# Kernel tuning notes

Measured on AMD Instinct MI355X. Metric: run time of the kernel, lower is better.

The kernel has to match this reference:

```python
import jax, jax.numpy as jnp
import numpy as np

N_NODES = 100000
N_EDGES = 1600000
DIM = 64          # num_features == hidden_dim
N_LAYERS = 5
N_GRAPHS = 1024
EMB = DIM * N_LAYERS  # 320
BN_EPS = 1e-5


def setup_inputs() -> dict:
    key = jax.random.key(0)
    ks = jax.random.split(key, 16)
    s = 0.05
    return {
        "x": jax.random.normal(ks[0], (N_NODES, DIM), dtype=jnp.float32),
        "edge_index": jax.random.randint(ks[1], (2, N_EDGES), 0, N_NODES, dtype=jnp.int32),
        "edge_weight": jax.random.uniform(ks[2], (N_EDGES,), dtype=jnp.float32),
        "batch": jnp.sort(jax.random.randint(ks[3], (N_NODES,), 0, N_GRAPHS, dtype=jnp.int32)),
        # stacked per-layer GIN MLP params: nn = Linear(d,d) -> ReLU -> Linear(d,d)
        "W1s": jax.random.normal(ks[4], (N_LAYERS, DIM, DIM), dtype=jnp.float32) * s,
        "b1s": jnp.zeros((N_LAYERS, DIM), dtype=jnp.float32),
        "W2s": jax.random.normal(ks[5], (N_LAYERS, DIM, DIM), dtype=jnp.float32) * s,
        "b2s": jnp.zeros((N_LAYERS, DIM), dtype=jnp.float32),
        # BatchNorm1d affine params (init: weight=1, bias=0)
        "gammas": jnp.ones((N_LAYERS, DIM), dtype=jnp.float32),
        "betas": jnp.zeros((N_LAYERS, DIM), dtype=jnp.float32),
        # projection head: Linear(EMB,EMB) -> ReLU -> Linear(EMB,EMB)
        "pW1": jax.random.normal(ks[6], (EMB, EMB), dtype=jnp.float32) * s,
        "pb1": jnp.zeros((EMB,), dtype=jnp.float32),
        "pW2": jax.random.normal(ks[7], (EMB, EMB), dtype=jnp.float32) * s,
        "pb2": jnp.zeros((EMB,), dtype=jnp.float32),
    }


def _encoder(x, src, dst, edge_weight, batch,
             W1s, b1s, W2s, b2s, gammas, betas):
    h = x
    pooled = []
    for i in range(N_LAYERS):
        # WGINConv (eps=0): h_out = nn(h + sum_{j->i} w_ij * h_j)
        msg = jax.ops.segment_sum(h[src] * edge_weight[:, None], dst,
                                  num_segments=N_NODES)  # [N, D]
        z = h + msg
        z = jnp.maximum(z @ W1s[i] + b1s[i], 0.0) @ W2s[i] + b2s[i]
        h = jnp.maximum(z, 0.0)  # F.relu after conv
        # BatchNorm1d (training mode: batch stats over nodes, biased var)
        mean = jnp.mean(h, axis=0)
        var = jnp.var(h, axis=0)
        h = (h - mean) * jax.lax.rsqrt(var + BN_EPS) * gammas[i] + betas[i]
        pooled.append(h)
    # global_mean_pool per layer, then concat along feature dim
    counts = jax.ops.segment_sum(jnp.ones((N_NODES,), h.dtype), batch,
                                 num_segments=N_GRAPHS)
    counts = jnp.maximum(counts, 1.0)[:, None]
    xpool = [jax.ops.segment_sum(h, batch, num_segments=N_GRAPHS) / counts
             for h in pooled]
    return jnp.concatenate(xpool, axis=1)  # [G, L*D]


def reference(x, edge_index, edge_weight, batch,
              W1s, b1s, W2s, b2s, gammas, betas,
              pW1, pb1, pW2, pb2):
    src, dst = edge_index[0], edge_index[1]
    y = _encoder(x, src, dst, edge_weight, batch,
                 W1s, b1s, W2s, b2s, gammas, betas)
    # proj_head: Linear -> ReLU -> Linear
    y = jnp.maximum(y @ pW1 + pb1, 0.0) @ pW2 + pb2
    return y
```

## Files before the change

### kernel.cpp

```cpp
#include <hip/hip_runtime.h>

#define NN 100000
#define NE 1600000
#define D 64
#define NL 5
#define NG 1024
#define EMBD 320
#define BN_EPS 1e-5f
#define SCAN_NB ((NN + 255) / 256)
#define GIN_NB ((NN + 63) / 64)

__global__ __launch_bounds__(256) void k_gbound(const int* __restrict__ batch,
                                                int* __restrict__ gstart) {
  int i = blockIdx.x * 256 + threadIdx.x;
  if (i >= NN) return;
  int b = batch[i];
  int bp = (i == 0) ? -1 : batch[i - 1];
  for (int g = bp + 1; g <= b; ++g) gstart[g] = i;
  if (i == NN - 1) {
    for (int g = b + 1; g <= NG; ++g) gstart[g] = NN;
  }
}

__global__ __launch_bounds__(256) void k_hist(const int* __restrict__ dst,
                                              int* __restrict__ deg) {
  int e = blockIdx.x * 256 + threadIdx.x;
  if (e < NE) atomicAdd(&deg[dst[e]], 1);
}

__global__ __launch_bounds__(256) void k_scan1(const int* __restrict__ deg,
                                               int* __restrict__ bsums) {
  __shared__ int sh[256];
  int i = blockIdx.x * 256 + threadIdx.x;
  sh[threadIdx.x] = (i < NN) ? deg[i] : 0;
  __syncthreads();
  for (int off = 128; off > 0; off >>= 1) {
    if (threadIdx.x < off) sh[threadIdx.x] += sh[threadIdx.x + off];
    __syncthreads();
  }
  if (threadIdx.x == 0) bsums[blockIdx.x] = sh[0];
}

__global__ __launch_bounds__(512) void k_scan2(int* __restrict__ bsums) {
  __shared__ int sh[512];
  int t = threadIdx.x;
  int v = (t < SCAN_NB) ? bsums[t] : 0;
  sh[t] = v;
  __syncthreads();
  for (int off = 1; off < 512; off <<= 1) {
    int u = (t >= off) ? sh[t - off] : 0;
    __syncthreads();
    sh[t] += u;
    __syncthreads();
  }
  if (t < SCAN_NB) bsums[t] = sh[t] - v;
}

__global__ __launch_bounds__(256) void k_scan3(int* __restrict__ row_ptr,
                                               int* __restrict__ cursor,
                                               const int* __restrict__ bsums) {
  __shared__ int sh[256];
  int t = threadIdx.x;
  int i = blockIdx.x * 256 + t;
  int v = (i < NN) ? row_ptr[i] : 0;
  sh[t] = v;
  __syncthreads();
  for (int off = 1; off < 256; off <<= 1) {
    int u = (t >= off) ? sh[t - off] : 0;
    __syncthreads();
    sh[t] += u;
    __syncthreads();
  }
  int excl = sh[t] - v + bsums[blockIdx.x];
  if (i < NN) {
    row_ptr[i] = excl;
    cursor[i] = excl;
    if (i == NN - 1) row_ptr[NN] = excl + v;
  }
}

__global__ __launch_bounds__(256) void k_fill(const int* __restrict__ src,
                                              const int* __restrict__ dst,
                                              const float* __restrict__ w,
                                              int* __restrict__ cursor,
                                              int2* __restrict__ epair) {
  int e = blockIdx.x * 256 + threadIdx.x;
  if (e >= NE) return;
  int slot = atomicAdd(&cursor[dst[e]], 1);
  int2 p;
  p.x = src[e];
  p.y = __float_as_int(w[e]);
  epair[slot] = p;
}

#define FMA4(A, V) \
  A.x = fmaf(V.x, we, A.x); A.y = fmaf(V.y, we, A.y); \
  A.z = fmaf(V.z, we, A.z); A.w = fmaf(V.w, we, A.w);

__global__ __launch_bounds__(256, 4) void k_gin(const float* __restrict__ h,
                                                float* __restrict__ gout,
                                                const int* __restrict__ row_ptr,
                                                const int2* __restrict__ epair,
                                                const float* __restrict__ W1,
                                                const float* __restrict__ b1,
                                                const float* __restrict__ W2,
                                                const float* __restrict__ b2,
                                                const float* __restrict__ statsP,
                                                const float* __restrict__ gammaP,
                                                const float* __restrict__ betaP,
                                                int useaff,
                                                float* __restrict__ statsL) {
  __shared__ float zin[64 * 65];
  __shared__ float sW[64 * 64];
  __shared__ float sb[64];
  __shared__ float wsumS[64];
  __shared__ float scA[64], sbA[64];
  __shared__ float sSf[256], sQf[256];
  const int t = threadIdx.x;
  const int nb = blockIdx.x * 64;
  const int nr = t >> 4, fc = t & 15;

  for (int i = t; i < 4096; i += 256) sW[i] = W1[i];
  if (t < 64) {
    sb[t] = b1[t];
    if (useaff) {
      float m = statsP[t] * (1.f / NN);
      float v = fmaxf(statsP[64 + t] * (1.f / NN) - m * m, 0.f);
      float sc = gammaP[t] * rsqrtf(v + BN_EPS);
      scA[t] = sc;
      sbA[t] = betaP[t] - m * sc;
    }
  }

  {
    const int nl = t >> 2;
    const int q = t & 3;
    const int n = nb + nl;
    float4 a0 = {0.f, 0.f, 0.f, 0.f}, a1 = a0, a2 = a0, a3 = a0;
    float wsum = 0.f;
    if (n < NN) {
      const int beg = row_ptr[n], end = row_ptr[n + 1];
      const float4* own = (const float4*)(h + (size_t)n * D) + q * 4;
      for (int i = beg; i < end; ++i) {
        const int2 pr = epair[i];
        const float we = __int_as_float(pr.y);
        const float4* hp = (const float4*)(h + (size_t)pr.x * D) + q * 4;
        float4 v0 = hp[0], v1 = hp[1], v2 = hp[2], v3 = hp[3];
        FMA4(a0, v0) FMA4(a1, v1) FMA4(a2, v2) FMA4(a3, v3)
        wsum += we;
      }
      float4 o0 = own[0], o1 = own[1], o2 = own[2], o3 = own[3];
      a0.x += o0.x; a0.y += o0.y; a0.z += o0.z; a0.w += o0.w;
      a1.x += o1.x; a1.y += o1.y; a1.z += o1.z; a1.w += o1.w;
      a2.x += o2.x; a2.y += o2.y; a2.z += o2.z; a2.w += o2.w;
      a3.x += o3.x; a3.y += o3.y; a3.z += o3.z; a3.w += o3.w;
    }
    float* zr = &zin[nl * 65 + q * 16];
    *(float4*)(zr + 0) = a0;
    *(float4*)(zr + 4) = a1;
    *(float4*)(zr + 8) = a2;
    *(float4*)(zr + 12) = a3;
    if (q == 0) wsumS[nl] = wsum;
  }
  __syncthreads();

  if (useaff) {
#pragma unroll
    for (int pass = 0; pass < 4; ++pass) {
      int idx = pass * 1024 + t * 4;
      int r = idx >> 6, c = idx & 63;
      float wp1 = 1.f + wsumS[r];
      float4 z = *(float4*)&zin[r * 65 + c];
      z.x = fmaf(z.x, scA[c + 0], sbA[c + 0] * wp1);
      z.y = fmaf(z.y, scA[c + 1], sbA[c + 1] * wp1);
      z.z = fmaf(z.z, scA[c + 2], sbA[c + 2] * wp1);
      z.w = fmaf(z.w, scA[c + 3], sbA[c + 3] * wp1);
      *(float4*)&zin[r * 65 + c] = z;
    }
    __syncthreads();
  }

#define GEMM_TILE(ACC)                                                        \
  {                                                                           \
    float4 bias = *(float4*)&sb[fc * 4];                                      \
    _Pragma("unroll") for (int i = 0; i < 4; ++i) ACC[i] = bias;              \
    _Pragma("unroll 4") for (int kc = 0; kc < 16; ++kc) {                     \
      float4 zv[4], wv[4];                                                    \
      _Pragma("unroll") for (int i = 0; i < 4; ++i)                           \
          zv[i] = *(float4*)&zin[(nr * 4 + i) * 65 + kc * 4];                 \
      _Pragma("unroll") for (int kk = 0; kk < 4; ++kk)                        \
          wv[kk] = *(float4*)&sW[(kc * 4 + kk) * 64 + fc * 4];                \
      _Pragma("unroll") for (int i = 0; i < 4; ++i) {                         \
        ACC[i].x = fmaf(zv[i].x, wv[0].x, ACC[i].x);                          \
        ACC[i].y = fmaf(zv[i].x, wv[0].y, ACC[i].y);                          \
        ACC[i].z = fmaf(zv[i].x, wv[0].z, ACC[i].z);                          \
        ACC[i].w = fmaf(zv[i].x, wv[0].w, ACC[i].w);                          \
        ACC[i].x = fmaf(zv[i].y, wv[1].x, ACC[i].x);                          \
        ACC[i].y = fmaf(zv[i].y, wv[1].y, ACC[i].y);                          \
        ACC[i].z = fmaf(zv[i].y, wv[1].z, ACC[i].z);                          \
        ACC[i].w = fmaf(zv[i].y, wv[1].w, ACC[i].w);                          \
        ACC[i].x = fmaf(zv[i].z, wv[2].x, ACC[i].x);                          \
        ACC[i].y = fmaf(zv[i].z, wv[2].y, ACC[i].y);                          \
        ACC[i].z = fmaf(zv[i].z, wv[2].z, ACC[i].z);                          \
        ACC[i].w = fmaf(zv[i].z, wv[2].w, ACC[i].w);                          \
        ACC[i].x = fmaf(zv[i].w, wv[3].x, ACC[i].x);                          \
        ACC[i].y = fmaf(zv[i].w, wv[3].y, ACC[i].y);                          \
        ACC[i].z = fmaf(zv[i].w, wv[3].z, ACC[i].z);                          \
        ACC[i].w = fmaf(zv[i].w, wv[3].w, ACC[i].w);                          \
      }                                                                       \
    }                                                                         \
    _Pragma("unroll") for (int i = 0; i < 4; ++i) {                           \
      ACC[i].x = fmaxf(ACC[i].x, 0.f);                                        \
      ACC[i].y = fmaxf(ACC[i].y, 0.f);                                        \
      ACC[i].z = fmaxf(ACC[i].z, 0.f);                                        \
      ACC[i].w = fmaxf(ACC[i].w, 0.f);                                        \
    }                                                                         \
  }

  float4 acc[4];
  GEMM_TILE(acc)
  __syncthreads();

#pragma unroll
  for (int i = 0; i < 4; ++i) *(float4*)&zin[(nr * 4 + i) * 65 + fc * 4] = acc[i];
  for (int i = t; i < 4096; i += 256) sW[i] = W2[i];
  if (t < 64) sb[t] = b2[t];
  __syncthreads();

  float4 acc2[4];
  GEMM_TILE(acc2)

  float4 s4 = {0.f, 0.f, 0.f, 0.f}, q4 = {0.f, 0.f, 0.f, 0.f};
#pragma unroll
  for (int i = 0; i < 4; ++i) {
    int n = nb + nr * 4 + i;
    if (n < NN) {
      *(float4*)(gout + (size_t)n * D + fc * 4) = acc2[i];
      s4.x += acc2[i].x; s4.y += acc2[i].y; s4.z += acc2[i].z; s4.w += acc2[i].w;
      q4.x = fmaf(acc2[i].x, acc2[i].x, q4.x);
      q4.y = fmaf(acc2[i].y, acc2[i].y, q4.y);
      q4.z = fmaf(acc2[i].z, acc2[i].z, q4.z);
      q4.w = fmaf(acc2[i].w, acc2[i].w, q4.w);
    }
  }
#pragma unroll
  for (int m = 16; m <= 32; m <<= 1) {
    s4.x += __shfl_xor(s4.x, m, 64); s4.y += __shfl_xor(s4.y, m, 64);
    s4.z += __shfl_xor(s4.z, m, 64); s4.w += __shfl_xor(s4.w, m, 64);
    q4.x += __shfl_xor(q4.x, m, 64); q4.y += __shfl_xor(q4.y, m, 64);
    q4.z += __shfl_xor(q4.z, m, 64); q4.w += __shfl_xor(q4.w, m, 64);
  }
  int wv_ = t >> 6;
  if ((t & 63) < 16) {
    *(float4*)&sSf[wv_ * 64 + fc * 4] = s4;
    *(float4*)&sQf[wv_ * 64 + fc * 4] = q4;
  }
  __syncthreads();
  if (t < 64) {
    float S = sSf[t] + sSf[64 + t] + sSf[128 + t] + sSf[192 + t];
    float Q = sQf[t] + sQf[64 + t] + sQf[128 + t] + sQf[192 + t];
    unsafeAtomicAdd(&statsL[t], S);
    unsafeAtomicAdd(&statsL[64 + t], Q);
  }
#undef GEMM_TILE
}

__global__ __launch_bounds__(256) void k_poolraw(const float* __restrict__ g_,
                                                 const int* __restrict__ gstart,
                                                 float* __restrict__ pooledraw,
                                                 int layer) {
  __shared__ float4 sh4[256];
  int g = blockIdx.x;
  int beg = gstart[g], end = gstart[g + 1];
  int p = threadIdx.x & 15, r = threadIdx.x >> 4;
  float4 s = {0.f, 0.f, 0.f, 0.f};
  for (int n = beg + r; n < end; n += 16) {
    float4 x = ((const float4*)(g_ + (size_t)n * D))[p];
    s.x += x.x; s.y += x.y; s.z += x.z; s.w += x.w;
  }
  sh4[threadIdx.x] = s;
  __syncthreads();
  if (threadIdx.x < 16) {
    float4 tot = {0.f, 0.f, 0.f, 0.f};
#pragma unroll
    for (int j = 0; j < 16; ++j) {
      float4 u = sh4[j * 16 + threadIdx.x];
      tot.x += u.x; tot.y += u.y; tot.z += u.z; tot.w += u.w;
    }
    int cnt = end - beg;
    float inv = 1.0f / (float)(cnt > 1 ? cnt : 1);
    float4 o = {tot.x * inv, tot.y * inv, tot.z * inv, tot.w * inv};
    ((float4*)(pooledraw + (size_t)g * EMBD + layer * D))[threadIdx.x] = o;
  }
}

__global__ __launch_bounds__(EMBD) void k_proj(const float* __restrict__ pooledraw,
                                               const float* __restrict__ stats,
                                               const float* __restrict__ gammas,
                                               const float* __restrict__ betas,
                                               const float* __restrict__ pW1,
                                               const float* __restrict__ pb1,
                                               const float* __restrict__ pW2,
                                               const float* __restrict__ pb2,
                                               float* __restrict__ out) {
  __shared__ float row[EMBD];
  __shared__ float y1[EMBD];
  int g = blockIdx.x, j = threadIdx.x;
  {
    int L = j >> 6, f = j & 63;
    float m = stats[L * 128 + f] * (1.f / NN);
    float v = fmaxf(stats[L * 128 + 64 + f] * (1.f / NN) - m * m, 0.f);
    float sc = gammas[L * D + f] * rsqrtf(v + BN_EPS);
    float sb = betas[L * D + f] - m * sc;
    row[j] = fmaf(pooledraw[(size_t)g * EMBD + j], sc, sb);
  }
  __syncthreads();
  float acc = pb1[j];
#pragma unroll 4
  for (int k = 0; k < EMBD; ++k) acc = fmaf(row[k], pW1[(size_t)k * EMBD + j], acc);
  y1[j] = fmaxf(acc, 0.f);
  __syncthreads();
  acc = pb2[j];
#pragma unroll 4
  for (int k = 0; k < EMBD; ++k) acc = fmaf(y1[k], pW2[(size_t)k * EMBD + j], acc);
  out[(size_t)g * EMBD + j] = acc;
}

extern "C" void kernel_launch(void* const* d_in, const int* in_sizes, int n_in,
                              void* d_out, int out_size, void* d_ws, size_t ws_size,
                              hipStream_t stream) {
  const float* x = (const float*)d_in[0];
  const int* ei = (const int*)d_in[1];
  const float* ew = (const float*)d_in[2];
  const int* batch = (const int*)d_in[3];
  const float* W1s = (const float*)d_in[4];
  const float* b1s = (const float*)d_in[5];
  const float* W2s = (const float*)d_in[6];
  const float* b2s = (const float*)d_in[7];
  const float* gammas = (const float*)d_in[8];
  const float* betas = (const float*)d_in[9];
  const float* pW1 = (const float*)d_in[10];
  const float* pb1 = (const float*)d_in[11];
  const float* pW2 = (const float*)d_in[12];
  const float* pb2 = (const float*)d_in[13];
  const int* srcv = ei;
  const int* dstv = ei + NE;

  char* ws = (char*)d_ws;
  float* gA = (float*)ws;
  float* gB = gA + (size_t)NN * D;
  float* stats = gB + (size_t)NN * D;
  float* pooledraw = stats + NL * 128;
  int* gstart = (int*)(pooledraw + (size_t)NG * EMBD);
  int* row_ptr = gstart + NG + 1;
  int* cursor = row_ptr + NN + 1;
  int2* epair = (int2*)(cursor + NN);
  int* bsums = (int*)(epair + NE);

  hipMemsetAsync(row_ptr, 0, (NN + 1) * sizeof(int), stream);
  hipMemsetAsync(stats, 0, NL * 128 * sizeof(float), stream);
  k_hist<<<(NE + 255) / 256, 256, 0, stream>>>(dstv, row_ptr);
  k_scan1<<<SCAN_NB, 256, 0, stream>>>(row_ptr, bsums);
  k_scan2<<<1, 512, 0, stream>>>(bsums);
  k_scan3<<<SCAN_NB, 256, 0, stream>>>(row_ptr, cursor, bsums);
  k_fill<<<(NE + 255) / 256, 256, 0, stream>>>(srcv, dstv, ew, cursor, epair);
  k_gbound<<<SCAN_NB, 256, 0, stream>>>(batch, gstart);

  const float* hin = x;
  float* gout = gA;
  for (int L = 0; L < NL; ++L) {
    k_gin<<<GIN_NB, 256, 0, stream>>>(hin, gout, row_ptr, epair,
                                      W1s + L * D * D, b1s + L * D,
                                      W2s + L * D * D, b2s + L * D,
                                      stats + (L > 0 ? (L - 1) * 128 : 0),
                                      gammas + (L > 0 ? (L - 1) * D : 0),
                                      betas + (L > 0 ? (L - 1) * D : 0),
                                      L > 0 ? 1 : 0,
                                      stats + L * 128);
    k_poolraw<<<NG, 256, 0, stream>>>(gout, gstart, pooledraw, L);
    hin = gout;
    gout = (gout == gA) ? gB : gA;
  }
  k_proj<<<NG, EMBD, 0, stream>>>(pooledraw, stats, gammas, betas,
                                  pW1, pb1, pW2, pb2, (float*)d_out);
}
```

Before: 830.7 us.

## Bucket edges by destination range before CSR fill; halve GIN weight smem for occupancy

CSR construction now runs as a two-level bucketed sort. Edges are first counted into 512-node buckets with shared-memory histograms, scattered into a temporary buffer with packed local dst bits, then per-bucket degrees and final slots are computed so that scattered global atomics and writes stay within a small address range. The GIN kernel loads each 64x64 weight matrix in two 32-row halves, reuses zin for the stat reduction, and raises the launch-bounds occupancy hint from 4 to 6 blocks per CU. This adds kernels, extra syncthreads and weight reloads, and the src packing relies on node ids fitting in 17 bits.

Measured after the change: 1.690 ms. 104% more time.

```diff
diff --git a/kernel.cpp b/kernel.cpp
--- a/kernel.cpp
+++ b/kernel.cpp
@@ -9,6 +9,8 @@
 #define BN_EPS 1e-5f
 #define SCAN_NB ((NN + 255) / 256)
 #define GIN_NB ((NN + 63) / 64)
+#define NBUCK 256
+#define NBUSED ((NN + 511) / 512)
 
 __global__ __launch_bounds__(256) void k_gbound(const int* __restrict__ batch,
                                                 int* __restrict__ gstart) {
@@ -22,10 +24,65 @@
   }
 }
 
-__global__ __launch_bounds__(256) void k_hist(const int* __restrict__ dst,
+__global__ __launch_bounds__(256) void k_bhist(const int* __restrict__ dst,
+                                               int* __restrict__ bhist) {
+  __shared__ int lh[NBUCK];
+  for (int i = threadIdx.x; i < NBUCK; i += 256) lh[i] = 0;
+  __syncthreads();
+  for (int e = blockIdx.x * 256 + threadIdx.x; e < NE; e += gridDim.x * 256)
+    atomicAdd(&lh[dst[e] >> 9], 1);
+  __syncthreads();
+  for (int i = threadIdx.x; i < NBUCK; i += 256)
+    if (lh[i]) atomicAdd(&bhist[i], lh[i]);
+}
+
+__global__ __launch_bounds__(NBUCK) void k_bscan(const int* __restrict__ bhist,
+                                                 int* __restrict__ boff,
+                                                 int* __restrict__ bcur) {
+  __shared__ int sh[NBUCK];
+  int t = threadIdx.x;
+  int v = bhist[t];
+  sh[t] = v;
+  __syncthreads();
+  for (int off = 1; off < NBUCK; off <<= 1) {
+    int u = (t >= off) ? sh[t - off] : 0;
+    __syncthreads();
+    sh[t] += u;
+    __syncthreads();
+  }
+  boff[t] = sh[t] - v;
+  bcur[t] = sh[t] - v;
+  if (t == NBUCK - 1) boff[NBUCK] = sh[t];
+}
+
+__global__ __launch_bounds__(256) void k_bfill(const int* __restrict__ src,
+                                               const int* __restrict__ dst,
+                                               const float* __restrict__ w,
+                                               int* __restrict__ bcur,
+                                               int2* __restrict__ tmp) {
+  for (int e = blockIdx.x * 256 + threadIdx.x; e < NE; e += gridDim.x * 256) {
+    int d = dst[e];
+    int slot = atomicAdd(&bcur[d >> 9], 1);
+    int2 p;
+    p.x = src[e] | ((d & 511) << 17);
+    p.y = __float_as_int(w[e]);
+    tmp[slot] = p;
+  }
+}
+
+__global__ __launch_bounds__(512) void k_bdeg(const int2* __restrict__ tmp,
+                                              const int* __restrict__ boff,
                                               int* __restrict__ deg) {
-  int e = blockIdx.x * 256 + threadIdx.x;
-  if (e < NE) atomicAdd(&deg[dst[e]], 1);
+  __shared__ int lh[512];
+  int b = blockIdx.x;
+  for (int i = threadIdx.x; i < 512; i += 512) lh[i] = 0;
+  __syncthreads();
+  int beg = boff[b], end = boff[b + 1];
+  for (int i = beg + threadIdx.x; i < end; i += 512)
+    atomicAdd(&lh[((unsigned)tmp[i].x) >> 17], 1);
+  __syncthreads();
+  int node = b * 512 + threadIdx.x;
+  if (node < NN) deg[node] = lh[threadIdx.x];
 }
 
 __global__ __launch_bounds__(256) void k_scan1(const int* __restrict__ deg,
@@ -79,25 +136,32 @@
   }
 }
 
-__global__ __launch_bounds__(256) void k_fill(const int* __restrict__ src,
-                                              const int* __restrict__ dst,
-                                              const float* __restrict__ w,
-                                              int* __restrict__ cursor,
-                                              int2* __restrict__ epair) {
-  int e = blockIdx.x * 256 + threadIdx.x;
-  if (e >= NE) return;
-  int slot = atomicAdd(&cursor[dst[e]], 1);
-  int2 p;
-  p.x = src[e];
-  p.y = __float_as_int(w[e]);
-  epair[slot] = p;
+__global__ __launch_bounds__(256) void k_fill2(const int2* __restrict__ tmp,
+                                               const int* __restrict__ boff,
+                                               int* __restrict__ cursor,
+                                               int2* __restrict__ epair) {
+  int b = blockIdx.x >> 2, part = blockIdx.x & 3;
+  int bbeg = boff[b], bend = boff[b + 1];
+  int cnt = bend - bbeg;
+  int beg = bbeg + (cnt * part) / 4;
+  int end = bbeg + (cnt * (part + 1)) / 4;
+  for (int i = beg + threadIdx.x; i < end; i += 256) {
+    int2 p = tmp[i];
+    int dl = ((unsigned)p.x) >> 17;
+    int d = b * 512 + dl;
+    int slot = atomicAdd(&cursor[d], 1);
+    int2 o;
+    o.x = p.x & 0x1FFFF;
+    o.y = p.y;
+    epair[slot] = o;
+  }
 }
 
 #define FMA4(A, V) \
   A.x = fmaf(V.x, we, A.x); A.y = fmaf(V.y, we, A.y); \
   A.z = fmaf(V.z, we, A.z); A.w = fmaf(V.w, we, A.w);
 
-__global__ __launch_bounds__(256, 4) void k_gin(const float* __restrict__ h,
+__global__ __launch_bounds__(256, 6) void k_gin(const float* __restrict__ h,
                                                 float* __restrict__ gout,
                                                 const int* __restrict__ row_ptr,
                                                 const int2* __restrict__ epair,
@@ -111,16 +175,15 @@
                                                 int useaff,
                                                 float* __restrict__ statsL) {
   __shared__ float zin[64 * 65];
-  __shared__ float sW[64 * 64];
+  __shared__ float sW[32 * 64];
   __shared__ float sb[64];
   __shared__ float wsumS[64];
   __shared__ float scA[64], sbA[64];
-  __shared__ float sSf[256], sQf[256];
   const int t = threadIdx.x;
   const int nb = blockIdx.x * 64;
   const int nr = t >> 4, fc = t & 15;
 
-  for (int i = t; i < 4096; i += 256) sW[i] = W1[i];
+  for (int i = t; i < 2048; i += 256) sW[i] = W1[i];
   if (t < 64) {
     sb[t] = b1[t];
     if (useaff) {
@@ -180,55 +243,73 @@
     __syncthreads();
   }
 
-#define GEMM_TILE(ACC)                                                        \
-  {                                                                           \
-    float4 bias = *(float4*)&sb[fc * 4];                                      \
-    _Pragma("unroll") for (int i = 0; i < 4; ++i) ACC[i] = bias;              \
-    _Pragma("unroll 4") for (int kc = 0; kc < 16; ++kc) {                     \
-      float4 zv[4], wv[4];                                                    \
-      _Pragma("unroll") for (int i = 0; i < 4; ++i)                           \
-          zv[i] = *(float4*)&zin[(nr * 4 + i) * 65 + kc * 4];                 \
-      _Pragma("unroll") for (int kk = 0; kk < 4; ++kk)                        \
-          wv[kk] = *(float4*)&sW[(kc * 4 + kk) * 64 + fc * 4];                \
-      _Pragma("unroll") for (int i = 0; i < 4; ++i) {                         \
-        ACC[i].x = fmaf(zv[i].x, wv[0].x, ACC[i].x);                          \
-        ACC[i].y = fmaf(zv[i].x, wv[0].y, ACC[i].y);                          \
-        ACC[i].z = fmaf(zv[i].x, wv[0].z, ACC[i].z);                          \
-        ACC[i].w = fmaf(zv[i].x, wv[0].w, ACC[i].w);                          \
-        ACC[i].x = fmaf(zv[i].y, wv[1].x, ACC[i].x);                          \
-        ACC[i].y = fmaf(zv[i].y, wv[1].y, ACC[i].y);                          \
-        ACC[i].z = fmaf(zv[i].y, wv[1].z, ACC[i].z);                          \
-        ACC[i].w = fmaf(zv[i].y, wv[1].w, ACC[i].w);                          \
-        ACC[i].x = fmaf(zv[i].z, wv[2].x, ACC[i].x);                          \
-        ACC[i].y = fmaf(zv[i].z, wv[2].y, ACC[i].y);                          \
-        ACC[i].z = fmaf(zv[i].z, wv[2].z, ACC[i].z);                          \
-        ACC[i].w = fmaf(zv[i].z, wv[2].w, ACC[i].w);                          \
-        ACC[i].x = fmaf(zv[i].w, wv[3].x, ACC[i].x);                          \
-        ACC[i].y = fmaf(zv[i].w, wv[3].y, ACC[i].y);                          \
-        ACC[i].z = fmaf(zv[i].w, wv[3].z, ACC[i].z);                          \
-        ACC[i].w = fmaf(zv[i].w, wv[3].w, ACC[i].w);                          \
-      }                                                                       \
+#define GEMM_HALF(ACC, KBASE)                                                 \
+  _Pragma("unroll 2") for (int kc = 0; kc < 8; ++kc) {                        \
+    float4 zv[4], wv[4];                                                      \
+    _Pragma("unroll") for (int i = 0; i < 4; ++i)                             \
+        zv[i] = *(float4*)&zin[(nr * 4 + i) * 65 + ((KBASE) + kc) * 4];       \
+    _Pragma("unroll") for (int kk = 0; kk < 4; ++kk)                          \
+        wv[kk] = *(float4*)&sW[(kc * 4 + kk) * 64 + fc * 4];                  \
+    _Pragma("unroll") for (int i = 0; i < 4; ++i) {                           \
+      ACC[i].x = fmaf(zv[i].x, wv[0].x, ACC[i].x);                            \
+      ACC[i].y = fmaf(zv[i].x, wv[0].y, ACC[i].y);                            \
+      ACC[i].z = fmaf(zv[i].x, wv[0].z, ACC[i].z);                            \
+      ACC[i].w = fmaf(zv[i].x, wv[0].w, ACC[i].w);                            \
+      ACC[i].x = fmaf(zv[i].y, wv[1].x, ACC[i].x);                            \
+      ACC[i].y = fmaf(zv[i].y, wv[1].y, ACC[i].y);                            \
+      ACC[i].z = fmaf(zv[i].y, wv[1].z, ACC[i].z);                            \
+      ACC[i].w = fmaf(zv[i].y, wv[1].w, ACC[i].w);                            \
+      ACC[i].x = fmaf(zv[i].z, wv[2].x, ACC[i].x);                            \
+      ACC[i].y = fmaf(zv[i].z, wv[2].y, ACC[i].y);                            \
+      ACC[i].z = fmaf(zv[i].z, wv[2].z, ACC[i].z);                            \
+      ACC[i].w = fmaf(zv[i].z, wv[2].w, ACC[i].w);                            \
+      ACC[i].x = fmaf(zv[i].w, wv[3].x, ACC[i].x);                            \
+      ACC[i].y = fmaf(zv[i].w, wv[3].y, ACC[i].y);                            \
+      ACC[i].z = fmaf(zv[i].w, wv[3].z, ACC[i].z);                            \
+      ACC[i].w = fmaf(zv[i].w, wv[3].w, ACC[i].w);                            \
     }                                                                         \
-    _Pragma("unroll") for (int i = 0; i < 4; ++i) {                           \
-      ACC[i].x = fmaxf(ACC[i].x, 0.f);                                        \
-      ACC[i].y = fmaxf(ACC[i].y, 0.f);                                        \
-      ACC[i].z = fmaxf(ACC[i].z, 0.f);                                        \
-      ACC[i].w = fmaxf(ACC[i].w, 0.f);                                        \
-    }                                                                         \
+  }
+
+#define RELU4(ACC)                                                            \
+  _Pragma("unroll") for (int i = 0; i < 4; ++i) {                             \
+    ACC[i].x = fmaxf(ACC[i].x, 0.f);                                          \
+    ACC[i].y = fmaxf(ACC[i].y, 0.f);                                          \
+    ACC[i].z = fmaxf(ACC[i].z, 0.f);                                          \
+    ACC[i].w = fmaxf(ACC[i].w, 0.f);                                          \
   }
 
   float4 acc[4];
-  GEMM_TILE(acc)
+  {
+    float4 bias = *(float4*)&sb[fc * 4];
+#pragma unroll
+    for (int i = 0; i < 4; ++i) acc[i] = bias;
+  }
+  GEMM_HALF(acc, 0)
+  __syncthreads();
+  for (int i = t; i < 2048; i += 256) sW[i] = W1[2048 + i];
+  __syncthreads();
+  GEMM_HALF(acc, 8)
+  RELU4(acc)
   __syncthreads();
 
 #pragma unroll
   for (int i = 0; i < 4; ++i) *(float4*)&zin[(nr * 4 + i) * 65 + fc * 4] = acc[i];
-  for (int i = t; i < 4096; i += 256) sW[i] = W2[i];
+  for (int i = t; i < 2048; i += 256) sW[i] = W2[i];
   if (t < 64) sb[t] = b2[t];
   __syncthreads();
 
   float4 acc2[4];
-  GEMM_TILE(acc2)
+  {
+    float4 bias = *(float4*)&sb[fc * 4];
+#pragma unroll
+    for (int i = 0; i < 4; ++i) acc2[i] = bias;
+  }
+  GEMM_HALF(acc2, 0)
+  __syncthreads();
+  for (int i = t; i < 2048; i += 256) sW[i] = W2[2048 + i];
+  __syncthreads();
+  GEMM_HALF(acc2, 8)
+  RELU4(acc2)
 
   float4 s4 = {0.f, 0.f, 0.f, 0.f}, q4 = {0.f, 0.f, 0.f, 0.f};
 #pragma unroll
@@ -250,19 +331,21 @@
     q4.x += __shfl_xor(q4.x, m, 64); q4.y += __shfl_xor(q4.y, m, 64);
     q4.z += __shfl_xor(q4.z, m, 64); q4.w += __shfl_xor(q4.w, m, 64);
   }
+  __syncthreads();
   int wv_ = t >> 6;
   if ((t & 63) < 16) {
-    *(float4*)&sSf[wv_ * 64 + fc * 4] = s4;
-    *(float4*)&sQf[wv_ * 64 + fc * 4] = q4;
+    *(float4*)&zin[wv_ * 64 + fc * 4] = s4;
+    *(float4*)&zin[256 + wv_ * 64 + fc * 4] = q4;
   }
   __syncthreads();
   if (t < 64) {
-    float S = sSf[t] + sSf[64 + t] + sSf[128 + t] + sSf[192 + t];
-    float Q = sQf[t] + sQf[64 + t] + sQf[128 + t] + sQf[192 + t];
+    float S = zin[t] + zin[64 + t] + zin[128 + t] + zin[192 + t];
+    float Q = zin[256 + t] + zin[320 + t] + zin[384 + t] + zin[448 + t];
     unsafeAtomicAdd(&statsL[t], S);
     unsafeAtomicAdd(&statsL[64 + t], Q);
   }
-#undef GEMM_TILE
+#undef GEMM_HALF
+#undef RELU4
 }
 
 __global__ __launch_bounds__(256) void k_poolraw(const float* __restrict__ g_,
@@ -356,14 +439,21 @@
   int* cursor = row_ptr + NN + 1;
   int2* epair = (int2*)(cursor + NN);
   int* bsums = (int*)(epair + NE);
-
-  hipMemsetAsync(row_ptr, 0, (NN + 1) * sizeof(int), stream);
+  int* bhist = bsums + SCAN_NB;
+  int* boff = bhist + NBUCK;
+  int* bcur = boff + NBUCK + 1;
+  int2* tmp = (int2*)gA;
+
+  hipMemsetAsync(bhist, 0, NBUCK * sizeof(int), stream);
   hipMemsetAsync(stats, 0, NL * 128 * sizeof(float), stream);
-  k_hist<<<(NE + 255) / 256, 256, 0, stream>>>(dstv, row_ptr);
+  k_bhist<<<1024, 256, 0, stream>>>(dstv, bhist);
+  k_bscan<<<1, NBUCK, 0, stream>>>(bhist, boff, bcur);
+  k_bfill<<<1024, 256, 0, stream>>>(srcv, dstv, ew, bcur, tmp);
+  k_bdeg<<<NBUSED, 512, 0, stream>>>(tmp, boff, row_ptr);
   k_scan1<<<SCAN_NB, 256, 0, stream>>>(row_ptr, bsums);
   k_scan2<<<1, 512, 0, stream>>>(bsums);
   k_scan3<<<SCAN_NB, 256, 0, stream>>>(row_ptr, cursor, bsums);
-  k_fill<<<(NE + 255) / 256, 256, 0, stream>>>(srcv, dstv, ew, cursor, epair);
+  k_fill2<<<NBUSED * 4, 256, 0, stream>>>(tmp, boff, cursor, epair);
   k_gbound<<<SCAN_NB, 256, 0, stream>>>(batch, gstart);
 
   const float* hin = x;
```
